# Kernel optimization log

Hardware: AMD Instinct MI355X
Metric: run time of the kernel (lower is better)

Reference implementation:

```python
import jax, jax.numpy as jnp
import numpy as np

B, L, ENC, DEC, ATT = 128, 196, 2048, 512, 512

def setup_inputs() -> dict:
    key = jax.random.key(0)
    ks = jax.random.split(key, 8)
    s_enc = 1.0 / np.sqrt(ENC)
    s_dec = 1.0 / np.sqrt(DEC)
    s_att = 1.0 / np.sqrt(ATT)
    return {
        "encoder_out": jax.random.normal(ks[0], (B, L, ENC), jnp.float32),
        "decoder_hidden": jax.random.normal(ks[1], (B, DEC), jnp.float32),
        "We": jax.random.uniform(ks[2], (ENC, ATT), jnp.float32, -s_enc, s_enc),
        "be": jax.random.uniform(ks[3], (ATT,), jnp.float32, -s_enc, s_enc),
        "Wd": jax.random.uniform(ks[4], (DEC, ATT), jnp.float32, -s_dec, s_dec),
        "bd": jax.random.uniform(ks[5], (ATT,), jnp.float32, -s_dec, s_dec),
        "wa": jax.random.uniform(ks[6], (ATT,), jnp.float32, -s_att, s_att),
        "ba": jax.random.uniform(ks[7], (), jnp.float32, -s_att, s_att),
    }

def reference(encoder_out, decoder_hidden, We, be, Wd, bd, wa, ba):
    # encoder_out: [B, L, ENC]; decoder_hidden: [B, DEC]
    enc_map = jnp.einsum('ble,ea->bla', encoder_out, We) + be          # [B, L, A]
    dec_map = decoder_hidden @ Wd + bd                                  # [B, A]
    scores = jnp.tanh(enc_map + dec_map[:, None, :]) @ wa + ba         # [B, L]
    alphas = jax.nn.softmax(scores, axis=1)                             # [B, L]
    context = jnp.einsum('bl,ble->be', alphas, encoder_out)             # [B, ENC]
    return (context, alphas)
```

## Files before the change

### kernel.cpp

```cpp
#include <hip/hip_runtime.h>

#define B_   128
#define L_   196
#define ENC_ 2048
#define DEC_ 512
#define ATT_ 512
#define M_   (B_ * L_)

typedef _Float16 f16x4 __attribute__((ext_vector_type(4)));
typedef _Float16 f16x8 __attribute__((ext_vector_type(8)));
typedef __fp16   h16x2 __attribute__((ext_vector_type(2)));
typedef float    f32x4 __attribute__((ext_vector_type(4)));

#define FENCE_LDS_BARRIER()                                        \
    do {                                                           \
        asm volatile("s_waitcnt lgkmcnt(0)" ::: "memory");         \
        __builtin_amdgcn_s_barrier();                              \
        __builtin_amdgcn_sched_barrier(0);                         \
    } while (0)


__global__ void wets_kernel(const float* __restrict__ We, _Float16* __restrict__ WeTs) {
    int u = blockIdx.x * 256 + threadIdx.x;
    int row = u & 127;
    int k8  = (u >> 7) & 3;
    int kt  = (u >> 9) & 63;
    int nt  = u >> 15;
    int n  = nt * 128 + row;
    int k0 = kt * 32 + k8 * 8;
    f16x8 h;
#pragma unroll
    for (int j = 0; j < 8; ++j) h[j] = (_Float16)We[(k0 + j) * ATT_ + n];
    *reinterpret_cast<f16x8*>(WeTs + (size_t)u * 8) = h;
}

__global__ void decmap_kernel(const float* __restrict__ dh, const float* __restrict__ Wd,
                              const float* __restrict__ bd, float* __restrict__ dec) {
    int b = blockIdx.x;
    int a = threadIdx.x;
    float acc = bd[a];
    const float* dhp = dh + b * DEC_;
#pragma unroll 8
    for (int k = 0; k < DEC_; ++k) acc += dhp[k] * Wd[k * ATT_ + a];
    dec[b * ATT_ + a] = acc;
}

__global__ __launch_bounds__(512, 1)
void gemm_score_kernel(const float* __restrict__ enc,
                       const _Float16* __restrict__ WeTs,
                       const float* __restrict__ be,
                       const float* __restrict__ wa,
                       const float* __restrict__ dec,
                       float* __restrict__ scores) {
    __shared__ _Float16 smem[3][4096];
    __shared__ float red[4][128];

    int mtile = blockIdx.x;
    int tid  = threadIdx.x;
    int lane = tid & 63, wid = tid >> 6;
    int wm = wid >> 2, wn = wid & 3;
    int l15 = lane & 15, lg = lane >> 4;

    int arowi = tid >> 2;
    int ac8   = tid & 3;
    const float* ag = enc + (size_t)(mtile * 128 + arowi) * ENC_ + ac8 * 8;
    int wa0 = (ac8 * 128 + (arowi ^ (2 * ac8))) * 8;

    const _Float16* bfr = WeTs +
        ((size_t)wn * 64 * 4 * 128 + (size_t)lg * 128 + l15) * 8;

    int afo = (lg * 128 + wm * 64 + (l15 ^ (2 * lg))) * 8;

    float4 areg0[2], areg1[2], areg2[2];
    f16x8  bf0[8], bf1[8];

    f32x4 acc[4][8];
#pragma unroll
    for (int mi = 0; mi < 4; ++mi)
#pragma unroll
        for (int ni = 0; ni < 8; ++ni) acc[mi][ni] = (f32x4){0.f, 0.f, 0.f, 0.f};

#define DEF_LOADA(S)                                                     \
    auto loadA##S = [&](int kt) {                                        \
        const float* a0 = ag + kt * 32;                                  \
        areg##S[0] = *reinterpret_cast<const float4*>(a0);               \
        areg##S[1] = *reinterpret_cast<const float4*>(a0 + 4);           \
    }
    DEF_LOADA(0); DEF_LOADA(1); DEF_LOADA(2);
#undef DEF_LOADA

#define DEF_LOADB(S)                                                     \
    auto loadB##S = [&](int kt) {                                        \
        const _Float16* s = bfr + (size_t)kt * 4096;                     \
        bf##S[0] = *reinterpret_cast<const f16x8*>(s + 0 * 128);         \
        bf##S[1] = *reinterpret_cast<const f16x8*>(s + 1 * 128);         \
        bf##S[2] = *reinterpret_cast<const f16x8*>(s + 2 * 128);         \
        bf##S[3] = *reinterpret_cast<const f16x8*>(s + 3 * 128);         \
        bf##S[4] = *reinterpret_cast<const f16x8*>(s + 4 * 128);         \
        bf##S[5] = *reinterpret_cast<const f16x8*>(s + 5 * 128);         \
        bf##S[6] = *reinterpret_cast<const f16x8*>(s + 6 * 128);         \
        bf##S[7] = *reinterpret_cast<const f16x8*>(s + 7 * 128);         \
    }
    DEF_LOADB(0); DEF_LOADB(1);
#undef DEF_LOADB

#define DEF_WRITEA(S)                                                    \
    auto writeA##S = [&](int buf) {                                      \
        _Float16* As = smem[buf];                                        \
        union { h16x2 h2[4]; f16x8 h8; } cv;                             \
        cv.h2[0] = __builtin_amdgcn_cvt_pkrtz(areg##S[0].x, areg##S[0].y); \
        cv.h2[1] = __builtin_amdgcn_cvt_pkrtz(areg##S[0].z, areg##S[0].w); \
        cv.h2[2] = __builtin_amdgcn_cvt_pkrtz(areg##S[1].x, areg##S[1].y); \
        cv.h2[3] = __builtin_amdgcn_cvt_pkrtz(areg##S[1].z, areg##S[1].w); \
        *reinterpret_cast<f16x8*>(As + wa0) = cv.h8;                     \
    }
    DEF_WRITEA(0); DEF_WRITEA(1); DEF_WRITEA(2);
#undef DEF_WRITEA

    auto compute = [&](const _Float16* As, const f16x8* bf) {
        f16x8 af[4];
#pragma unroll
        for (int mi = 0; mi < 4; ++mi)
            af[mi] = *reinterpret_cast<const f16x8*>(As + afo + mi * 128);
        __builtin_amdgcn_s_setprio(1);
#pragma unroll
        for (int mi = 0; mi < 4; ++mi)
#pragma unroll
            for (int ni = 0; ni < 8; ++ni)
                acc[mi][ni] = __builtin_amdgcn_mfma_f32_16x16x32_f16(
                    af[mi], bf[ni], acc[mi][ni], 0, 0, 0);
        __builtin_amdgcn_s_setprio(0);
    };

#define PHASE(KT, S, WS, BS, CBS, RBUF, WBUF)                            \
    do {                                                                 \
        int ka = (KT) + 3 < 64 ? (KT) + 3 : 63;                          \
        int kb = (KT) + 1 < 64 ? (KT) + 1 : 63;                          \
        loadB##BS(kb);                                                   \
        __builtin_amdgcn_sched_barrier(0);                               \
        loadA##S(ka);                                                    \
        writeA##WS(WBUF);                                                \
        FENCE_LDS_BARRIER();                                             \
        compute(smem[RBUF], bf##CBS);                                    \
    } while (0)

    loadB0(0);
    __builtin_amdgcn_sched_barrier(0);
    loadA0(0);
    loadA1(1);
    loadA2(2);
    writeA0(0);
    FENCE_LDS_BARRIER();

    for (int kt6 = 0; kt6 < 10; ++kt6) {
        int kt = kt6 * 6;
        PHASE(kt + 0, 0, 1, 1, 0, 0, 1);
        PHASE(kt + 1, 1, 2, 0, 1, 1, 2);
        PHASE(kt + 2, 2, 0, 1, 0, 2, 0);
        PHASE(kt + 3, 0, 1, 0, 1, 0, 1);
        PHASE(kt + 4, 1, 2, 1, 0, 1, 2);
        PHASE(kt + 5, 2, 0, 0, 1, 2, 0);
    }
    PHASE(60, 0, 1, 1, 0, 0, 1);
    PHASE(61, 1, 2, 0, 1, 1, 2);
    PHASE(62, 2, 0, 1, 0, 2, 0);
    PHASE(63, 0, 1, 0, 1, 0, 1);
#undef PHASE

    float rsum[4][4];
#pragma unroll
    for (int mi = 0; mi < 4; ++mi)
#pragma unroll
        for (int j = 0; j < 4; ++j) rsum[mi][j] = 0.f;

    int rb = mtile * 128 + wm * 64;
#pragma unroll
    for (int ni = 0; ni < 8; ++ni) {
        int n = wn * 128 + ni * 16 + l15;
        float wav = wa[n];
        float bev = be[n];
#pragma unroll
        for (int mi = 0; mi < 4; ++mi) {
#pragma unroll
            for (int j = 0; j < 4; ++j) {
                int row = rb + mi * 16 + lg * 4 + j;
                int b = row / L_;
                float x = acc[mi][ni][j] + bev + dec[b * ATT_ + n];
                float e = __expf(2.0f * x);
                float t = 1.0f - 2.0f / (e + 1.0f);
                rsum[mi][j] += t * wav;
            }
        }
    }
#pragma unroll
    for (int mi = 0; mi < 4; ++mi) {
#pragma unroll
        for (int j = 0; j < 4; ++j) {
            float v = rsum[mi][j];
            v += __shfl_xor(v, 1);
            v += __shfl_xor(v, 2);
            v += __shfl_xor(v, 4);
            v += __shfl_xor(v, 8);
            if (l15 == 0) red[wn][wm * 64 + mi * 16 + lg * 4 + j] = v;
        }
    }
    __syncthreads();
    if (tid < 128)
        scores[mtile * 128 + tid] = red[0][tid] + red[1][tid] + red[2][tid] + red[3][tid];
}

__global__ void softmax_kernel(const float* __restrict__ scores, float* __restrict__ alphas) {
    int b = blockIdx.x, t = threadIdx.x;
    int lane = t & 63, wid = t >> 6;
    __shared__ float red[4];
    float s = 0.f, val = -1e30f;
    if (t < L_) {
        s = scores[b * L_ + t];
        val = s;
    }
    float m = val;
#pragma unroll
    for (int off = 1; off < 64; off <<= 1) m = fmaxf(m, __shfl_xor(m, off));
    if (lane == 0) red[wid] = m;
    __syncthreads();
    m = fmaxf(fmaxf(red[0], red[1]), fmaxf(red[2], red[3]));
    float e = (t < L_) ? __expf(s - m) : 0.f;
    float sum = e;
#pragma unroll
    for (int off = 1; off < 64; off <<= 1) sum += __shfl_xor(sum, off);
    __syncthreads();
    if (lane == 0) red[wid] = sum;
    __syncthreads();
    sum = red[0] + red[1] + red[2] + red[3];
    if (t < L_) alphas[b * L_ + t] = e / sum;
}

__global__ void context_kernel(const float* __restrict__ enc, const float* __restrict__ alphas,
                               float* __restrict__ ctx) {
    int b = blockIdx.x >> 2;
    int ec = blockIdx.x & 3;
    int e = ec * 512 + threadIdx.x * 2;
    const float* ep = enc + (size_t)b * L_ * ENC_ + e;
    const float* ap = alphas + b * L_;
    float ax = 0.f, ay = 0.f;
#pragma unroll 4
    for (int l = 0; l < L_; ++l) {
        float a = ap[l];
        float2 v = *reinterpret_cast<const float2*>(ep + (size_t)l * ENC_);
        ax += a * v.x;
        ay += a * v.y;
    }
    float2 r; r.x = ax; r.y = ay;
    *reinterpret_cast<float2*>(&ctx[b * ENC_ + e]) = r;
}

extern "C" void kernel_launch(void* const* d_in, const int* in_sizes, int n_in,
                              void* d_out, int out_size, void* d_ws, size_t ws_size,
                              hipStream_t stream) {
    const float* enc = (const float*)d_in[0];
    const float* dh  = (const float*)d_in[1];
    const float* We  = (const float*)d_in[2];
    const float* be  = (const float*)d_in[3];
    const float* Wd  = (const float*)d_in[4];
    const float* bd  = (const float*)d_in[5];
    const float* wa  = (const float*)d_in[6];

    float* out    = (float*)d_out;
    float* ctx    = out;
    float* alphas = out + B_ * ENC_;

    char* ws = (char*)d_ws;
    float*    dec     = (float*)ws;
    _Float16* WeTs    = (_Float16*)(ws + 262144);
    float*    scores  = (float*)(ws + 262144 + 2097152);

    hipLaunchKernelGGL(wets_kernel,       dim3(512),  dim3(256), 0, stream, We, WeTs);
    hipLaunchKernelGGL(decmap_kernel,     dim3(128),  dim3(512), 0, stream, dh, Wd, bd, dec);
    hipLaunchKernelGGL(gemm_score_kernel, dim3(196),  dim3(512), 0, stream, enc, WeTs, be, wa, dec, scores);
    hipLaunchKernelGGL(softmax_kernel,    dim3(128),  dim3(256), 0, stream, scores, alphas);
    hipLaunchKernelGGL(context_kernel,    dim3(512),  dim3(256), 0, stream, enc, alphas, ctx);
}
```

Measured before the change: 143.2 us.

## Restructure GEMM pipeline to double-buffered LDS with compute before A store

Replaces the triple-buffered LDS and three-register A prefetch pipeline with a double-buffered scheme. The A tile is loaded two steps ahead, and the LDS write happens after the MFMA block so global latency is hidden behind compute. It also switches launch bounds to waves_per_eu(2,2), which lets the compiler use a different register budget. Fewer prefetch registers and LDS buffers are meant to cut pressure, at the cost of a shorter prefetch distance and an extra barrier per k-step.

```diff
diff --git a/kernel.cpp b/kernel.cpp
--- a/kernel.cpp
+++ b/kernel.cpp
@@ -7,7 +7,6 @@
 #define ATT_ 512
 #define M_   (B_ * L_)
 
-typedef _Float16 f16x4 __attribute__((ext_vector_type(4)));
 typedef _Float16 f16x8 __attribute__((ext_vector_type(8)));
 typedef __fp16   h16x2 __attribute__((ext_vector_type(2)));
 typedef float    f32x4 __attribute__((ext_vector_type(4)));
@@ -45,14 +44,14 @@
     dec[b * ATT_ + a] = acc;
 }
 
-__global__ __launch_bounds__(512, 1)
+__global__ __launch_bounds__(512) __attribute__((amdgpu_waves_per_eu(2, 2)))
 void gemm_score_kernel(const float* __restrict__ enc,
                        const _Float16* __restrict__ WeTs,
                        const float* __restrict__ be,
                        const float* __restrict__ wa,
                        const float* __restrict__ dec,
                        float* __restrict__ scores) {
-    __shared__ _Float16 smem[3][4096];
+    __shared__ _Float16 As[2][4096];
     __shared__ float red[4][128];
 
     int mtile = blockIdx.x;
@@ -71,7 +70,7 @@
 
     int afo = (lg * 128 + wm * 64 + (l15 ^ (2 * lg))) * 8;
 
-    float4 areg0[2], areg1[2], areg2[2];
+    float4 areg0[2], areg1[2];
     f16x8  bf0[8], bf1[8];
 
     f32x4 acc[4][8];
@@ -86,7 +85,7 @@
         areg##S[0] = *reinterpret_cast<const float4*>(a0);               \
         areg##S[1] = *reinterpret_cast<const float4*>(a0 + 4);           \
     }
-    DEF_LOADA(0); DEF_LOADA(1); DEF_LOADA(2);
+    DEF_LOADA(0); DEF_LOADA(1);
 #undef DEF_LOADA
 
 #define DEF_LOADB(S)                                                     \
@@ -106,66 +105,58 @@
 
 #define DEF_WRITEA(S)                                                    \
     auto writeA##S = [&](int buf) {                                      \
-        _Float16* As = smem[buf];                                        \
         union { h16x2 h2[4]; f16x8 h8; } cv;                             \
         cv.h2[0] = __builtin_amdgcn_cvt_pkrtz(areg##S[0].x, areg##S[0].y); \
         cv.h2[1] = __builtin_amdgcn_cvt_pkrtz(areg##S[0].z, areg##S[0].w); \
         cv.h2[2] = __builtin_amdgcn_cvt_pkrtz(areg##S[1].x, areg##S[1].y); \
         cv.h2[3] = __builtin_amdgcn_cvt_pkrtz(areg##S[1].z, areg##S[1].w); \
-        *reinterpret_cast<f16x8*>(As + wa0) = cv.h8;                     \
-    }
-    DEF_WRITEA(0); DEF_WRITEA(1); DEF_WRITEA(2);
+        *reinterpret_cast<f16x8*>(&As[buf][wa0]) = cv.h8;                \
+    }
+    DEF_WRITEA(0); DEF_WRITEA(1);
 #undef DEF_WRITEA
 
-    auto compute = [&](const _Float16* As, const f16x8* bf) {
-        f16x8 af[4];
-#pragma unroll
-        for (int mi = 0; mi < 4; ++mi)
-            af[mi] = *reinterpret_cast<const f16x8*>(As + afo + mi * 128);
-        __builtin_amdgcn_s_setprio(1);
-#pragma unroll
-        for (int mi = 0; mi < 4; ++mi)
-#pragma unroll
-            for (int ni = 0; ni < 8; ++ni)
-                acc[mi][ni] = __builtin_amdgcn_mfma_f32_16x16x32_f16(
-                    af[mi], bf[ni], acc[mi][ni], 0, 0, 0);
-        __builtin_amdgcn_s_setprio(0);
-    };
-
-#define PHASE(KT, S, WS, BS, CBS, RBUF, WBUF)                            \
+#define COMPUTE(BUF, BF)                                                 \
     do {                                                                 \
-        int ka = (KT) + 3 < 64 ? (KT) + 3 : 63;                          \
-        int kb = (KT) + 1 < 64 ? (KT) + 1 : 63;                          \
-        loadB##BS(kb);                                                   \
-        __builtin_amdgcn_sched_barrier(0);                               \
-        loadA##S(ka);                                                    \
-        writeA##WS(WBUF);                                                \
-        FENCE_LDS_BARRIER();                                             \
-        compute(smem[RBUF], bf##CBS);                                    \
+        f16x8 af[4];                                                     \
+        _Pragma("unroll")                                                \
+        for (int mi = 0; mi < 4; ++mi)                                   \
+            af[mi] = *reinterpret_cast<const f16x8*>(&As[BUF][afo + mi * 128]); \
+        __builtin_amdgcn_s_setprio(1);                                   \
+        _Pragma("unroll")                                                \
+        for (int mi = 0; mi < 4; ++mi)                                   \
+            _Pragma("unroll")                                            \
+            for (int ni = 0; ni < 8; ++ni)                               \
+                acc[mi][ni] = __builtin_amdgcn_mfma_f32_16x16x32_f16(    \
+                    af[mi], BF[ni], acc[mi][ni], 0, 0, 0);               \
+        __builtin_amdgcn_s_setprio(0);                                   \
     } while (0)
 
     loadB0(0);
     __builtin_amdgcn_sched_barrier(0);
     loadA0(0);
     loadA1(1);
-    loadA2(2);
     writeA0(0);
     FENCE_LDS_BARRIER();
 
-    for (int kt6 = 0; kt6 < 10; ++kt6) {
-        int kt = kt6 * 6;
-        PHASE(kt + 0, 0, 1, 1, 0, 0, 1);
-        PHASE(kt + 1, 1, 2, 0, 1, 1, 2);
-        PHASE(kt + 2, 2, 0, 1, 0, 2, 0);
-        PHASE(kt + 3, 0, 1, 0, 1, 0, 1);
-        PHASE(kt + 4, 1, 2, 1, 0, 1, 2);
-        PHASE(kt + 5, 2, 0, 0, 1, 2, 0);
-    }
-    PHASE(60, 0, 1, 1, 0, 0, 1);
-    PHASE(61, 1, 2, 0, 1, 1, 2);
-    PHASE(62, 2, 0, 1, 0, 2, 0);
-    PHASE(63, 0, 1, 0, 1, 0, 1);
-#undef PHASE
+    for (int kt2 = 0; kt2 < 32; ++kt2) {
+        int kt = kt2 * 2;
+        loadB1(kt + 1);
+        __builtin_amdgcn_sched_barrier(0);
+        if (kt2 < 31) loadA0(kt + 2);
+        COMPUTE(0, bf0);
+        writeA1(1);
+        FENCE_LDS_BARRIER();
+        {
+            int kb = kt + 2 < 64 ? kt + 2 : 63;
+            loadB0(kb);
+        }
+        __builtin_amdgcn_sched_barrier(0);
+        if (kt2 < 31) loadA1(kt + 3);
+        COMPUTE(1, bf1);
+        if (kt2 < 31) writeA0(0);
+        FENCE_LDS_BARRIER();
+    }
+#undef COMPUTE
 
     float rsum[4][4];
 #pragma unroll
@@ -272,11 +263,11 @@
     char* ws = (char*)d_ws;
     float*    dec     = (float*)ws;
     _Float16* WeTs    = (_Float16*)(ws + 262144);
-    float*    scores  = (float*)(ws + 262144 + 2097152);
-
-    hipLaunchKernelGGL(wets_kernel,       dim3(512),  dim3(256), 0, stream, We, WeTs);
-    hipLaunchKernelGGL(decmap_kernel,     dim3(128),  dim3(512), 0, stream, dh, Wd, bd, dec);
-    hipLaunchKernelGGL(gemm_score_kernel, dim3(196),  dim3(512), 0, stream, enc, WeTs, be, wa, dec, scores);
-    hipLaunchKernelGGL(softmax_kernel,    dim3(128),  dim3(256), 0, stream, scores, alphas);
-    hipLaunchKernelGGL(context_kernel,    dim3(512),  dim3(256), 0, stream, enc, alphas, ctx);
-}
+    float*    scores  = (float*)(ws + 2359296);
+
+    hipLaunchKernelGGL(wets_kernel,       dim3(512), dim3(256), 0, stream, We, WeTs);
+    hipLaunchKernelGGL(decmap_kernel,     dim3(128), dim3(512), 0, stream, dh, Wd, bd, dec);
+    hipLaunchKernelGGL(gemm_score_kernel, dim3(196), dim3(512), 0, stream, enc, WeTs, be, wa, dec, scores);
+    hipLaunchKernelGGL(softmax_kernel,    dim3(128), dim3(256), 0, stream, scores, alphas);
+    hipLaunchKernelGGL(context_kernel,    dim3(512), dim3(256), 0, stream, enc, alphas, ctx);
+}
```

After: 142.0 us. No clear change (-0.8%).
